# Kernel tuning notes

Hardware: AMD Instinct MI355X
Metric: run time of the kernel (lower is better)

## Reference

```python
import jax, jax.numpy as jnp
import numpy as np

ALPHA = 0.2          # LeakyReLU negative slope
NEG_BIG = -9e15      # mask value from original code


def setup_inputs() -> dict:
    key = jax.random.key(0)
    k1, k2, k3, k4 = jax.random.split(key, 4)
    B, N, F_in, F_out = 16, 1024, 256, 256
    x = jax.random.normal(k1, (B, N, F_in), dtype=jnp.float32)
    adj = jax.random.randint(k2, (B, N, N), 0, 2, dtype=jnp.int32)
    # xavier-uniform-like scales
    W = jax.random.normal(k3, (F_in, F_out), dtype=jnp.float32) * np.sqrt(2.0 / (F_in + F_out))
    a = jax.random.normal(k4, (2 * F_out, 1), dtype=jnp.float32) * np.sqrt(2.0 / (2 * F_out + 1))
    return {"x": x, "adj": adj, "W": W, "a": a}


def reference(x, adj, W, a):
    # x: [B,N,Fin], adj: [B,N,N] (int mask), W: [Fin,Fout], a: [2*Fout,1]
    F_out = a.shape[0] // 2
    h = jnp.einsum("bni,io->bno", x, W)            # [B,N,Fout]
    # Decompose a into left/right halves: e_ij = lrelu(a_l.h_i + a_r.h_j)
    a_l = a[:F_out, 0]                               # [Fout]
    a_r = a[F_out:, 0]                               # [Fout]
    el = h @ a_l                                     # [B,N] score contribution of target i
    er = h @ a_r                                     # [B,N] score contribution of source j
    e = jax.nn.leaky_relu(el[:, :, None] + er[:, None, :], ALPHA)  # [B,N,N]
    e = jnp.where(adj > 0, e, NEG_BIG)
    attn = jax.nn.softmax(e, axis=-1)                # masked softmax over neighbors j
    # weighted sum of neighbor features; concat with n_heads=1 is identity
    return jnp.einsum("bij,bjo->bio", attn, h)       # [B,N,Fout]
```

## Files before the change

kernel.cpp:

```cpp
#include <hip/hip_runtime.h>
#include <stdint.h>

#define ALPHA 0.2f
#define NEG_BIG -9000000000000000.0f

typedef __attribute__((ext_vector_type(8))) short bf16x8;
typedef __attribute__((ext_vector_type(8))) unsigned short u16x8;
typedef __attribute__((ext_vector_type(4))) float f32x4;

__device__ __forceinline__ unsigned short f2bf(float f) {
    unsigned int u = __float_as_uint(f);
    u += 0x7fffu + ((u >> 16) & 1u);
    return (unsigned short)(u >> 16);
}
__device__ __forceinline__ float bf2f(unsigned short h) {
    return __uint_as_float(((unsigned int)h) << 16);
}

__device__ __forceinline__ void gload_lds16(const void* g, void* l) {
    __builtin_amdgcn_global_load_lds(
        (const __attribute__((address_space(1))) unsigned int*)g,
        (__attribute__((address_space(3))) unsigned int*)l, 16, 0, 0);
}

__global__ void wt_kernel(const float* __restrict__ W, float* __restrict__ Wt) {
    int o = blockIdx.x, k = threadIdx.x;
    Wt[o * 256 + k] = W[k * 256 + o];
}

__global__ __launch_bounds__(256) void gemm_f32in(
    const float* __restrict__ A,
    const float* __restrict__ Bt,
    unsigned short* __restrict__ C,
    int M, int N, int K,
    long long sA, long long sB, long long sC)
{
    __shared__ __align__(16) float As[128 * 32];
    __shared__ __align__(16) float Bs[128 * 32];

    const int tid = threadIdx.x;
    const int w = tid >> 6;
    const int l = tid & 63;
    const int q = l >> 4;
    const int ml = l & 15;
    const int wm = (w >> 1) * 64;
    const int wn = (w & 1) * 64;

    const int m0 = blockIdx.y * 128;
    const int n0 = blockIdx.x * 128;
    const float* Ab = A + (size_t)blockIdx.z * sA;
    const float* Bb = Bt + (size_t)blockIdx.z * sB;
    unsigned short* Cb = C + (size_t)blockIdx.z * sC;

    f32x4 acc[4][4];
    for (int i = 0; i < 4; ++i)
        for (int j = 0; j < 4; ++j) {
            f32x4 z = {0.f, 0.f, 0.f, 0.f};
            acc[i][j] = z;
        }

    for (int k0 = 0; k0 < K; k0 += 32) {
        for (int c = 0; c < 4; ++c) {
            const int cb = c * 256 + (w << 6);
            const int chunk = cb + l;
            const int r  = chunk >> 3;
            const int co = (chunk & 7) << 2;
            gload_lds16(Ab + (size_t)(m0 + r) * K + k0 + co, As + cb * 4);
            gload_lds16(Bb + (size_t)(n0 + r) * K + k0 + co, Bs + cb * 4);
        }
        __syncthreads();

        bf16x8 aF[4], bF[4];
        for (int mt = 0; mt < 4; ++mt) {
            const float* ap = As + (wm + mt * 16 + ml) * 32 + q * 8;
#pragma unroll
            for (int u = 0; u < 8; ++u) aF[mt][u] = (short)f2bf(ap[u]);
        }
        for (int nt = 0; nt < 4; ++nt) {
            const float* bp = Bs + (wn + nt * 16 + ml) * 32 + q * 8;
#pragma unroll
            for (int u = 0; u < 8; ++u) bF[nt][u] = (short)f2bf(bp[u]);
        }
        for (int mt = 0; mt < 4; ++mt)
            for (int nt = 0; nt < 4; ++nt)
                acc[mt][nt] = __builtin_amdgcn_mfma_f32_16x16x32_bf16(
                    aF[mt], bF[nt], acc[mt][nt], 0, 0, 0);
        __syncthreads();
    }

    for (int mt = 0; mt < 4; ++mt)
        for (int nt = 0; nt < 4; ++nt) {
            const int gn = n0 + wn + nt * 16 + ml;
            for (int r = 0; r < 4; ++r) {
                const int gm = m0 + wm + mt * 16 + q * 4 + r;
                Cb[(size_t)gm * N + gn] = f2bf(acc[mt][nt][r]);
            }
        }
}

__global__ __launch_bounds__(256) void eler_kernel(
    const unsigned short* __restrict__ h_t,
    const float* __restrict__ a,
    float* __restrict__ el, float* __restrict__ er)
{
    const int gi = blockIdx.x * 256 + threadIdx.x;
    const int b = gi >> 10, ii = gi & 1023;
    const unsigned short* hb = h_t + ((size_t)b * 256) * 1024 + ii;
    float sl = 0.f, sr = 0.f;
#pragma unroll 4
    for (int o = 0; o < 256; ++o) {
        const float v = bf2f(hb[(size_t)o * 1024]);
        sl += v * a[o];
        sr += v * a[256 + o];
    }
    el[gi] = sl;
    er[gi] = sr;
}

__global__ __launch_bounds__(256) void fused_attn(
    const int* __restrict__ adj,
    const float* __restrict__ el,
    const float* __restrict__ er,
    const unsigned short* __restrict__ h_t,
    float* __restrict__ out)
{
    __shared__ float er_s[1024];
    __shared__ float el_s[64];
    __shared__ float c_s[64];
    __shared__ unsigned char nib[64][256];
    __shared__ __align__(16) unsigned short Hs[256 * 32];
    __shared__ __align__(16) unsigned short Ps[64 * 32];

    const int tid = threadIdx.x;
    const int w = tid >> 6, l = tid & 63;
    const int q = l >> 4, ml = l & 15;
    const int b = blockIdx.y;
    const int i0 = blockIdx.x * 64;

    *(float4*)(er_s + tid * 4) = *(const float4*)(er + b * 1024 + tid * 4);
    if (tid < 64) el_s[tid] = el[b * 1024 + i0 + tid];
    __syncthreads();

    for (int rr = 0; rr < 16; ++rr) {
        const int row = w * 16 + rr;
        const int* arow = adj + (size_t)(b * 1024 + i0 + row) * 1024;
        const float eli = el_s[row];
        float ev[16];
        float m = -3.0e38f;
#pragma unroll
        for (int it = 0; it < 4; ++it) {
            const int j = it * 256 + l * 4;
            const int4 av = *(const int4*)(arow + j);
            float e0 = eli + er_s[j + 0]; e0 = e0 > 0.f ? e0 : ALPHA * e0; e0 = av.x > 0 ? e0 : NEG_BIG;
            float e1 = eli + er_s[j + 1]; e1 = e1 > 0.f ? e1 : ALPHA * e1; e1 = av.y > 0 ? e1 : NEG_BIG;
            float e2 = eli + er_s[j + 2]; e2 = e2 > 0.f ? e2 : ALPHA * e2; e2 = av.z > 0 ? e2 : NEG_BIG;
            float e3 = eli + er_s[j + 3]; e3 = e3 > 0.f ? e3 : ALPHA * e3; e3 = av.w > 0 ? e3 : NEG_BIG;
            ev[it * 4 + 0] = e0; ev[it * 4 + 1] = e1;
            ev[it * 4 + 2] = e2; ev[it * 4 + 3] = e3;
            m = fmaxf(m, fmaxf(fmaxf(e0, e1), fmaxf(e2, e3)));
            nib[row][it * 64 + l] =
                (unsigned char)((av.x > 0) | ((av.y > 0) << 1) |
                                ((av.z > 0) << 2) | ((av.w > 0) << 3));
        }
#pragma unroll
        for (int off = 32; off >= 1; off >>= 1) m = fmaxf(m, __shfl_xor(m, off));
        float s = 0.f;
#pragma unroll
        for (int u = 0; u < 16; ++u) s += __expf(ev[u] - m);
#pragma unroll
        for (int off = 32; off >= 1; off >>= 1) s += __shfl_xor(s, off);
        if (l == 0) c_s[row] = m + __logf(s);
    }
    __syncthreads();

    const int ib = tid >> 2;
    const int js = (tid & 3) * 8;
    const float eli_b = el_s[ib];
    const float ci = c_s[ib];

    f32x4 acc[4][4];
    for (int i = 0; i < 4; ++i)
        for (int j = 0; j < 4; ++j) {
            f32x4 z = {0.f, 0.f, 0.f, 0.f};
            acc[i][j] = z;
        }

    const unsigned short* hb = h_t + (size_t)b * 262144;

    for (int j0 = 0; j0 < 1024; j0 += 32) {
        for (int c = 0; c < 4; ++c) {
            const int cb = c * 256 + (w << 6);
            const int chunk = cb + l;
            const int r  = chunk >> 2;
            const int co = (chunk & 3) << 3;
            gload_lds16(hb + (size_t)r * 1024 + j0 + co, Hs + cb * 8);
        }
        {
            const unsigned byte_i = (unsigned)(j0 + js) >> 2;
            const unsigned v0 = nib[ib][byte_i];
            const unsigned v1 = nib[ib][byte_i + 1];
            const unsigned v = v0 | (v1 << 4);
            u16x8 pvv;
#pragma unroll
            for (int u = 0; u < 8; ++u) {
                float e = eli_b + er_s[j0 + js + u];
                e = e > 0.f ? e : ALPHA * e;
                const float p = ((v >> u) & 1u) ? __expf(e - ci) : 0.f;
                pvv[u] = f2bf(p);
            }
            *(u16x8*)(Ps + ib * 32 + js) = pvv;
        }
        __syncthreads();

        bf16x8 aF[4], bF[4];
        for (int mt = 0; mt < 4; ++mt)
            aF[mt] = *(const bf16x8*)(Ps + (mt * 16 + ml) * 32 + q * 8);
        for (int nt = 0; nt < 4; ++nt)
            bF[nt] = *(const bf16x8*)(Hs + ((w << 6) + nt * 16 + ml) * 32 + q * 8);
        for (int mt = 0; mt < 4; ++mt)
            for (int nt = 0; nt < 4; ++nt)
                acc[mt][nt] = __builtin_amdgcn_mfma_f32_16x16x32_bf16(
                    aF[mt], bF[nt], acc[mt][nt], 0, 0, 0);
        __syncthreads();
    }

    float* ob = out + (size_t)b * 262144;
    for (int mt = 0; mt < 4; ++mt)
        for (int nt = 0; nt < 4; ++nt) {
            const int gn = (w << 6) + nt * 16 + ml;
            for (int r = 0; r < 4; ++r) {
                const int gm = i0 + mt * 16 + q * 4 + r;
                ob[(size_t)gm * 256 + gn] = acc[mt][nt][r];
            }
        }
}

extern "C" void kernel_launch(void* const* d_in, const int* in_sizes, int n_in,
                              void* d_out, int out_size, void* d_ws, size_t ws_size,
                              hipStream_t stream) {
    const float* x   = (const float*)d_in[0];
    const int*   adj = (const int*)d_in[1];
    const float* W   = (const float*)d_in[2];
    const float* a   = (const float*)d_in[3];
    float* out = (float*)d_out;

    char* ws = (char*)d_ws;
    float* Wt           = (float*)(ws);
    unsigned short* h_t = (unsigned short*)(ws + 262144);
    float* el           = (float*)(ws + 8650752);
    float* er           = (float*)(ws + 8716288);

    wt_kernel<<<dim3(256), dim3(256), 0, stream>>>(W, Wt);

    gemm_f32in<<<dim3(8, 2, 16), dim3(256), 0, stream>>>(
        Wt, x, h_t, 256, 1024, 256, 0LL, 1024LL * 256, 256LL * 1024);

    eler_kernel<<<dim3(64), dim3(256), 0, stream>>>(h_t, a, el, er);

    fused_attn<<<dim3(16, 16), dim3(256), 0, stream>>>(adj, el, er, h_t, out);
}
```

Baseline: 188.7 us.

## Split attention into mask/softmax-stat kernel and PV kernel; compute el/er from x

Precomputes W·a so el/er are dot products of x with two 256-vectors instead of strided reads of bf16 h. The fused attention kernel is split in two. A highly parallel mask kernel reads adj once, computes the per-row log-sum-exp and writes a packed 16-bit adjacency bitmask. A PV kernel with 32-row tiles then reuses that mask to build bf16 probabilities and run the MFMA matmul. This spreads the adj scan across far more blocks and doubles PV-grid occupancy, but adds launches and halves the reuse of each H tile per block, so h is reloaded twice as often.

```diff
diff --git a/kernel.cpp b/kernel.cpp
--- a/kernel.cpp
+++ b/kernel.cpp
@@ -13,9 +13,6 @@
     u += 0x7fffu + ((u >> 16) & 1u);
     return (unsigned short)(u >> 16);
 }
-__device__ __forceinline__ float bf2f(unsigned short h) {
-    return __uint_as_float(((unsigned int)h) << 16);
-}
 
 __device__ __forceinline__ void gload_lds16(const void* g, void* l) {
     __builtin_amdgcn_global_load_lds(
@@ -23,9 +20,44 @@
         (__attribute__((address_space(3))) unsigned int*)l, 16, 0, 0);
 }
 
-__global__ void wt_kernel(const float* __restrict__ W, float* __restrict__ Wt) {
-    int o = blockIdx.x, k = threadIdx.x;
-    Wt[o * 256 + k] = W[k * 256 + o];
+__global__ void wt_wa_kernel(const float* __restrict__ W,
+                             const float* __restrict__ a,
+                             float* __restrict__ Wt,
+                             float* __restrict__ wa) {
+    const int t = threadIdx.x;
+    if (blockIdx.x < 256) {
+        const int o = blockIdx.x;
+        Wt[o * 256 + t] = W[t * 256 + o];
+    } else {
+        float sl = 0.f, sr = 0.f;
+        const float* wr = W + t * 256;
+        for (int o = 0; o < 256; ++o) {
+            const float wv = wr[o];
+            sl += wv * a[o];
+            sr += wv * a[256 + o];
+        }
+        wa[t] = sl;
+        wa[256 + t] = sr;
+    }
+}
+
+__global__ __launch_bounds__(256) void eler2_kernel(
+    const float* __restrict__ x, const float* __restrict__ wa,
+    float* __restrict__ el, float* __restrict__ er)
+{
+    const int w = threadIdx.x >> 6, l = threadIdx.x & 63;
+    const int r = blockIdx.x * 4 + w;
+    const float4 xv = *(const float4*)(x + (size_t)r * 256 + l * 4);
+    const float4 al = *(const float4*)(wa + l * 4);
+    const float4 ar = *(const float4*)(wa + 256 + l * 4);
+    float sl = xv.x * al.x + xv.y * al.y + xv.z * al.z + xv.w * al.w;
+    float sr = xv.x * ar.x + xv.y * ar.y + xv.z * ar.z + xv.w * ar.w;
+#pragma unroll
+    for (int off = 32; off >= 1; off >>= 1) {
+        sl += __shfl_xor(sl, off);
+        sr += __shfl_xor(sr, off);
+    }
+    if (l == 0) { el[r] = sl; er[r] = sr; }
 }
 
 __global__ __launch_bounds__(256) void gemm_f32in(
@@ -98,88 +130,86 @@
         }
 }
 
-__global__ __launch_bounds__(256) void eler_kernel(
-    const unsigned short* __restrict__ h_t,
-    const float* __restrict__ a,
-    float* __restrict__ el, float* __restrict__ er)
-{
-    const int gi = blockIdx.x * 256 + threadIdx.x;
-    const int b = gi >> 10, ii = gi & 1023;
-    const unsigned short* hb = h_t + ((size_t)b * 256) * 1024 + ii;
-    float sl = 0.f, sr = 0.f;
-#pragma unroll 4
-    for (int o = 0; o < 256; ++o) {
-        const float v = bf2f(hb[(size_t)o * 1024]);
-        sl += v * a[o];
-        sr += v * a[256 + o];
-    }
-    el[gi] = sl;
-    er[gi] = sr;
-}
-
-__global__ __launch_bounds__(256) void fused_attn(
+__global__ __launch_bounds__(256) void mask_kernel(
     const int* __restrict__ adj,
     const float* __restrict__ el,
     const float* __restrict__ er,
+    float* __restrict__ c,
+    unsigned short* __restrict__ pk16)
+{
+    __shared__ unsigned char nibs[4][256];
+
+    const int w = threadIdx.x >> 6, l = threadIdx.x & 63;
+    const int row = blockIdx.x * 4 + w;
+    const int b = row >> 10;
+    const int* arow = adj + (size_t)row * 1024;
+    const float* erb = er + (b << 10);
+    const float eli = el[row];
+
+    float ev[16];
+    float m = -3.0e38f;
+#pragma unroll
+    for (int it = 0; it < 4; ++it) {
+        const int j = it * 256 + l * 4;
+        const int4 av = *(const int4*)(arow + j);
+        const float4 erv = *(const float4*)(erb + j);
+        float e0 = eli + erv.x; e0 = e0 > 0.f ? e0 : ALPHA * e0; e0 = av.x > 0 ? e0 : NEG_BIG;
+        float e1 = eli + erv.y; e1 = e1 > 0.f ? e1 : ALPHA * e1; e1 = av.y > 0 ? e1 : NEG_BIG;
+        float e2 = eli + erv.z; e2 = e2 > 0.f ? e2 : ALPHA * e2; e2 = av.z > 0 ? e2 : NEG_BIG;
+        float e3 = eli + erv.w; e3 = e3 > 0.f ? e3 : ALPHA * e3; e3 = av.w > 0 ? e3 : NEG_BIG;
+        ev[it * 4 + 0] = e0; ev[it * 4 + 1] = e1;
+        ev[it * 4 + 2] = e2; ev[it * 4 + 3] = e3;
+        m = fmaxf(m, fmaxf(fmaxf(e0, e1), fmaxf(e2, e3)));
+        nibs[w][it * 64 + l] =
+            (unsigned char)((av.x > 0) | ((av.y > 0) << 1) |
+                            ((av.z > 0) << 2) | ((av.w > 0) << 3));
+    }
+#pragma unroll
+    for (int off = 32; off >= 1; off >>= 1) m = fmaxf(m, __shfl_xor(m, off));
+    float s = 0.f;
+#pragma unroll
+    for (int u = 0; u < 16; ++u) s += __expf(ev[u] - m);
+#pragma unroll
+    for (int off = 32; off >= 1; off >>= 1) s += __shfl_xor(s, off);
+    if (l == 0) c[row] = m + __logf(s);
+
+    const unsigned nr = *(const unsigned int*)(&nibs[w][l * 4]);
+    const unsigned short mask16 =
+        (unsigned short)((nr & 0xFu) | ((nr >> 4) & 0xF0u) |
+                         ((nr >> 8) & 0xF00u) | ((nr >> 12) & 0xF000u));
+    pk16[(size_t)row * 64 + l] = mask16;
+}
+
+__global__ __launch_bounds__(256) void pv_kernel(
+    const unsigned short* __restrict__ pk16,
+    const float* __restrict__ el,
+    const float* __restrict__ er,
+    const float* __restrict__ c,
     const unsigned short* __restrict__ h_t,
     float* __restrict__ out)
 {
     __shared__ float er_s[1024];
-    __shared__ float el_s[64];
-    __shared__ float c_s[64];
-    __shared__ unsigned char nib[64][256];
+    __shared__ __align__(16) unsigned short pk_s[32 * 64];
     __shared__ __align__(16) unsigned short Hs[256 * 32];
-    __shared__ __align__(16) unsigned short Ps[64 * 32];
+    __shared__ __align__(16) unsigned short Ps[32 * 40];
 
     const int tid = threadIdx.x;
     const int w = tid >> 6, l = tid & 63;
     const int q = l >> 4, ml = l & 15;
     const int b = blockIdx.y;
-    const int i0 = blockIdx.x * 64;
-
-    *(float4*)(er_s + tid * 4) = *(const float4*)(er + b * 1024 + tid * 4);
-    if (tid < 64) el_s[tid] = el[b * 1024 + i0 + tid];
+    const int i0 = blockIdx.x * 32;
+
+    *(float4*)(er_s + tid * 4) = *(const float4*)(er + (b << 10) + tid * 4);
+    *(u16x8*)(pk_s + tid * 8) =
+        *(const u16x8*)(pk16 + ((size_t)(b << 10) + i0) * 64 + tid * 8);
+    const int ib = tid >> 3;
+    const int js = (tid & 7) * 4;
+    const float eli_b = el[(b << 10) + i0 + ib];
+    const float ci = c[(b << 10) + i0 + ib];
     __syncthreads();
 
-    for (int rr = 0; rr < 16; ++rr) {
-        const int row = w * 16 + rr;
-        const int* arow = adj + (size_t)(b * 1024 + i0 + row) * 1024;
-        const float eli = el_s[row];
-        float ev[16];
-        float m = -3.0e38f;
-#pragma unroll
-        for (int it = 0; it < 4; ++it) {
-            const int j = it * 256 + l * 4;
-            const int4 av = *(const int4*)(arow + j);
-            float e0 = eli + er_s[j + 0]; e0 = e0 > 0.f ? e0 : ALPHA * e0; e0 = av.x > 0 ? e0 : NEG_BIG;
-            float e1 = eli + er_s[j + 1]; e1 = e1 > 0.f ? e1 : ALPHA * e1; e1 = av.y > 0 ? e1 : NEG_BIG;
-            float e2 = eli + er_s[j + 2]; e2 = e2 > 0.f ? e2 : ALPHA * e2; e2 = av.z > 0 ? e2 : NEG_BIG;
-            float e3 = eli + er_s[j + 3]; e3 = e3 > 0.f ? e3 : ALPHA * e3; e3 = av.w > 0 ? e3 : NEG_BIG;
-            ev[it * 4 + 0] = e0; ev[it * 4 + 1] = e1;
-            ev[it * 4 + 2] = e2; ev[it * 4 + 3] = e3;
-            m = fmaxf(m, fmaxf(fmaxf(e0, e1), fmaxf(e2, e3)));
-            nib[row][it * 64 + l] =
-                (unsigned char)((av.x > 0) | ((av.y > 0) << 1) |
-                                ((av.z > 0) << 2) | ((av.w > 0) << 3));
-        }
-#pragma unroll
-        for (int off = 32; off >= 1; off >>= 1) m = fmaxf(m, __shfl_xor(m, off));
-        float s = 0.f;
-#pragma unroll
-        for (int u = 0; u < 16; ++u) s += __expf(ev[u] - m);
-#pragma unroll
-        for (int off = 32; off >= 1; off >>= 1) s += __shfl_xor(s, off);
-        if (l == 0) c_s[row] = m + __logf(s);
-    }
-    __syncthreads();
-
-    const int ib = tid >> 2;
-    const int js = (tid & 3) * 8;
-    const float eli_b = el_s[ib];
-    const float ci = c_s[ib];
-
-    f32x4 acc[4][4];
-    for (int i = 0; i < 4; ++i)
+    f32x4 acc[2][4];
+    for (int i = 0; i < 2; ++i)
         for (int j = 0; j < 4; ++j) {
             f32x4 z = {0.f, 0.f, 0.f, 0.f};
             acc[i][j] = z;
@@ -188,36 +218,36 @@
     const unsigned short* hb = h_t + (size_t)b * 262144;
 
     for (int j0 = 0; j0 < 1024; j0 += 32) {
-        for (int c = 0; c < 4; ++c) {
-            const int cb = c * 256 + (w << 6);
+        for (int cc = 0; cc < 4; ++cc) {
+            const int cb = cc * 256 + (w << 6);
             const int chunk = cb + l;
             const int r  = chunk >> 2;
             const int co = (chunk & 3) << 3;
             gload_lds16(hb + (size_t)r * 1024 + j0 + co, Hs + cb * 8);
         }
         {
-            const unsigned byte_i = (unsigned)(j0 + js) >> 2;
-            const unsigned v0 = nib[ib][byte_i];
-            const unsigned v1 = nib[ib][byte_i + 1];
-            const unsigned v = v0 | (v1 << 4);
-            u16x8 pvv;
-#pragma unroll
-            for (int u = 0; u < 8; ++u) {
-                float e = eli_b + er_s[j0 + js + u];
-                e = e > 0.f ? e : ALPHA * e;
-                const float p = ((v >> u) & 1u) ? __expf(e - ci) : 0.f;
-                pvv[u] = f2bf(p);
-            }
-            *(u16x8*)(Ps + ib * 32 + js) = pvv;
-        }
-        __syncthreads();
-
-        bf16x8 aF[4], bF[4];
-        for (int mt = 0; mt < 4; ++mt)
-            aF[mt] = *(const bf16x8*)(Ps + (mt * 16 + ml) * 32 + q * 8);
+            const unsigned hw = pk_s[ib * 64 + ((j0 + js) >> 4)];
+            const unsigned v = (hw >> ((j0 + js) & 15)) & 0xFu;
+            ushort4 pvv;
+            float e;
+            e = eli_b + er_s[j0 + js + 0]; e = e > 0.f ? e : ALPHA * e;
+            pvv.x = (v & 1u) ? f2bf(__expf(e - ci)) : (unsigned short)0;
+            e = eli_b + er_s[j0 + js + 1]; e = e > 0.f ? e : ALPHA * e;
+            pvv.y = (v & 2u) ? f2bf(__expf(e - ci)) : (unsigned short)0;
+            e = eli_b + er_s[j0 + js + 2]; e = e > 0.f ? e : ALPHA * e;
+            pvv.z = (v & 4u) ? f2bf(__expf(e - ci)) : (unsigned short)0;
+            e = eli_b + er_s[j0 + js + 3]; e = e > 0.f ? e : ALPHA * e;
+            pvv.w = (v & 8u) ? f2bf(__expf(e - ci)) : (unsigned short)0;
+            *(ushort4*)(Ps + ib * 40 + js) = pvv;
+        }
+        __syncthreads();
+
+        bf16x8 aF[2], bF[4];
+        for (int mt = 0; mt < 2; ++mt)
+            aF[mt] = *(const bf16x8*)(Ps + (mt * 16 + ml) * 40 + q * 8);
         for (int nt = 0; nt < 4; ++nt)
             bF[nt] = *(const bf16x8*)(Hs + ((w << 6) + nt * 16 + ml) * 32 + q * 8);
-        for (int mt = 0; mt < 4; ++mt)
+        for (int mt = 0; mt < 2; ++mt)
             for (int nt = 0; nt < 4; ++nt)
                 acc[mt][nt] = __builtin_amdgcn_mfma_f32_16x16x32_bf16(
                     aF[mt], bF[nt], acc[mt][nt], 0, 0, 0);
@@ -225,7 +255,7 @@
     }
 
     float* ob = out + (size_t)b * 262144;
-    for (int mt = 0; mt < 4; ++mt)
+    for (int mt = 0; mt < 2; ++mt)
         for (int nt = 0; nt < 4; ++nt) {
             const int gn = (w << 6) + nt * 16 + ml;
             for (int r = 0; r < 4; ++r) {
@@ -245,17 +275,22 @@
     float* out = (float*)d_out;
 
     char* ws = (char*)d_ws;
-    float* Wt           = (float*)(ws);
-    unsigned short* h_t = (unsigned short*)(ws + 262144);
-    float* el           = (float*)(ws + 8650752);
-    float* er           = (float*)(ws + 8716288);
-
-    wt_kernel<<<dim3(256), dim3(256), 0, stream>>>(W, Wt);
+    float* Wt             = (float*)(ws);
+    float* wa             = (float*)(ws + 262144);
+    unsigned short* h_t   = (unsigned short*)(ws + 264192);
+    float* el             = (float*)(ws + 8652800);
+    float* er             = (float*)(ws + 8718336);
+    float* c              = (float*)(ws + 8783872);
+    unsigned short* pk16  = (unsigned short*)(ws + 8849408);
+
+    wt_wa_kernel<<<dim3(257), dim3(256), 0, stream>>>(W, a, Wt, wa);
+
+    eler2_kernel<<<dim3(4096), dim3(256), 0, stream>>>(x, wa, el, er);
 
     gemm_f32in<<<dim3(8, 2, 16), dim3(256), 0, stream>>>(
         Wt, x, h_t, 256, 1024, 256, 0LL, 1024LL * 256, 256LL * 1024);
 
-    eler_kernel<<<dim3(64), dim3(256), 0, stream>>>(h_t, a, el, er);
-
-    fused_attn<<<dim3(16, 16), dim3(256), 0, stream>>>(adj, el, er, h_t, out);
-}
+    mask_kernel<<<dim3(4096), dim3(256), 0, stream>>>(adj, el, er, c, pk16);
+
+    pv_kernel<<<dim3(32, 16), dim3(256), 0, stream>>>(pk16, el, er, c, h_t, out);
+}
```

Measured after the change: 163.6 us. -13.3%, faster.
